# Kernel optimization log

Measured on AMD Instinct MI355X. Metric: run time of the kernel, lower is better.

## Reference

```python
import jax, jax.numpy as jnp
import numpy as np

N = 50000
E = 800000
F_IN = 128
H = 64
C = 10
BN_EPS = 1e-5


def _glorot(key, shape):
    fan_in = shape[0]
    return jax.random.normal(key, shape, dtype=jnp.float32) / jnp.sqrt(jnp.float32(fan_in))


def setup_inputs() -> dict:
    key = jax.random.key(0)
    ks = jax.random.split(key, 16)
    inp = {
        "x": jax.random.normal(ks[0], (N, F_IN), dtype=jnp.float32),
        "edge_index": jax.random.randint(ks[1], (2, E), 0, N, dtype=jnp.int64),
    }
    # GINConv layer params: eps (train_eps=True, init 0), 2-layer MLP, BN affine
    dims = [(F_IN, H), (H, H), (H, H)]
    for i, (din, dout) in enumerate(dims, start=1):
        k1, k2 = jax.random.split(ks[1 + i], 2)
        inp[f"eps{i}"] = jnp.float32(0.0)
        inp[f"w{i}a"] = _glorot(k1, (din, H))
        inp[f"b{i}a"] = jnp.zeros((H,), jnp.float32)
        inp[f"w{i}b"] = _glorot(k2, (H, H))
        inp[f"b{i}b"] = jnp.zeros((H,), jnp.float32)
        inp[f"g{i}"] = jnp.ones((H,), jnp.float32)
        inp[f"be{i}"] = jnp.zeros((H,), jnp.float32)
    inp["lin_w"] = _glorot(ks[10], (H, C))
    inp["lin_b"] = jnp.zeros((C,), jnp.float32)
    return inp


def _gin_conv(x, src, dst, eps, wa, ba, wb, bb, g, be):
    # sum-aggregate neighbor features: scatter-add x[src] into dst rows
    agg = jax.ops.segment_sum(x[src], dst, num_segments=N)
    h = (1.0 + eps) * x + agg
    # MLP: Linear-ReLU-Linear-ReLU-BatchNorm1d (training-mode batch stats)
    h = jax.nn.relu(h @ wa + ba)
    h = jax.nn.relu(h @ wb + bb)
    mean = jnp.mean(h, axis=0)
    var = jnp.var(h, axis=0)
    return (h - mean) * jax.lax.rsqrt(var + BN_EPS) * g + be


def reference(x, edge_index,
              eps1, w1a, b1a, w1b, b1b, g1, be1,
              eps2, w2a, b2a, w2b, b2b, g2, be2,
              eps3, w3a, b3a, w3b, b3b, g3, be3,
              lin_w, lin_b):
    src, dst = edge_index[0], edge_index[1]
    h = jax.nn.relu(_gin_conv(x, src, dst, eps1, w1a, b1a, w1b, b1b, g1, be1))
    h = jax.nn.relu(_gin_conv(h, src, dst, eps2, w2a, b2a, w2b, b2b, g2, be2))
    h = jax.nn.relu(_gin_conv(h, src, dst, eps3, w3a, b3a, w3b, b3b, g3, be3))
    return h @ lin_w + lin_b
```

## Files before the change

### kernel.cpp

```cpp
#include <hip/hip_runtime.h>
#include <hip/hip_fp16.h>

#define NN 50000
#define NGROUP 3125
#define NCHUNK 391
#define CHCAP 3072
#define SLAB 8192
#define BN_EPS 1e-5f

typedef unsigned int uint;
typedef unsigned short ushort;
typedef _Float16 half8 __attribute__((ext_vector_type(8)));
typedef float floatx4 __attribute__((ext_vector_type(4)));

__device__ __forceinline__ int aswz(int slot) { return slot ^ ((slot >> 4) & 7); }

__device__ __forceinline__ float h_lo(uint u) {
    return __half2float(__ushort_as_half((ushort)(u & 0xFFFFu)));
}
__device__ __forceinline__ float h_hi(uint u) {
    return __half2float(__ushort_as_half((ushort)(u >> 16)));
}
__device__ __forceinline__ void unpack8(uint4 v, float* f) {
    f[0] = h_lo(v.x); f[1] = h_hi(v.x);
    f[2] = h_lo(v.y); f[3] = h_hi(v.y);
    f[4] = h_lo(v.z); f[5] = h_hi(v.z);
    f[6] = h_lo(v.w); f[7] = h_hi(v.w);
}

__global__ __launch_bounds__(256) void sortA_kernel(
    const int* __restrict__ ei, int* __restrict__ gcur,
    uint* __restrict__ bucket, int E)
{
    __shared__ int s_hist[NCHUNK];
    __shared__ int s_offs[NCHUNK];
    __shared__ int s_cur[NCHUNK];
    __shared__ int s_gb[NCHUNK];
    __shared__ int s_scanA[512], s_scanB[512];
    __shared__ uint s_sorted[SLAB];

    const int tid  = threadIdx.x;
    const int base = blockIdx.x * SLAB;
    const int cnt  = min(SLAB, E - base);

    for (int i = tid; i < NCHUNK; i += 256) s_hist[i] = 0;
    __syncthreads();

    uint pk[SLAB / 256];
    int nloc = 0;
    for (int i = tid; i < cnt; i += 256) {
        int src = ei[base + i];
        int dst = ei[E + base + i];
        int c = dst >> 7;
        pk[nloc++] = (uint)src | ((uint)(dst & 127) << 16) | ((uint)c << 23);
        atomicAdd(&s_hist[c], 1);
    }
    __syncthreads();
    for (int i = tid; i < 512; i += 256) s_scanA[i] = (i < NCHUNK) ? s_hist[i] : 0;
    __syncthreads();
    int* sa = s_scanA; int* sb = s_scanB;
    for (int off = 1; off < 512; off <<= 1) {
        for (int i = tid; i < 512; i += 256)
            sb[i] = sa[i] + ((i >= off) ? sa[i - off] : 0);
        __syncthreads();
        int* t = sa; sa = sb; sb = t;
    }
    for (int i = tid; i < NCHUNK; i += 256) {
        int excl = sa[i] - s_hist[i];
        s_offs[i] = excl;
        s_cur[i]  = excl;
    }
    __syncthreads();
    for (int k = 0; k < nloc; k++) {
        int c = pk[k] >> 23;
        int pos = atomicAdd(&s_cur[c], 1);
        s_sorted[pos] = pk[k];
    }
    __syncthreads();
    for (int c = tid; c < NCHUNK; c += 256) {
        int n = s_hist[c];
        s_gb[c] = n ? atomicAdd(&gcur[c], n) : 0;
    }
    __syncthreads();
    for (int i = tid; i < cnt; i += 256) {
        uint v = s_sorted[i];
        int c = v >> 23;
        int li = i - s_offs[c];
        bucket[(size_t)c * CHCAP + s_gb[c] + li] = v;
    }
}

__global__ __launch_bounds__(256) void fillB_kernel(
    const uint* __restrict__ bucket, const int* __restrict__ gcur,
    int* __restrict__ rowPtr, int* __restrict__ csr_src)
{
    __shared__ int s_hist[128];
    __shared__ int s_excl[128];
    __shared__ int s_cur[128];
    __shared__ int s_ws[4];
    __shared__ int s_base;
    const int c = blockIdx.x;
    const int tid = threadIdx.x;
    const int cnt = gcur[c];
    const int row0 = c * 128;

    int part = 0;
    for (int i = tid; i < c; i += 256) part += gcur[i];
    #pragma unroll
    for (int off = 32; off >= 1; off >>= 1) part += __shfl_down(part, off, 64);
    if ((tid & 63) == 0) s_ws[tid >> 6] = part;
    if (tid < 128) s_hist[tid] = 0;
    __syncthreads();
    if (tid == 0) s_base = s_ws[0] + s_ws[1] + s_ws[2] + s_ws[3];
    __syncthreads();
    const int base = s_base;
    if (tid == 0 && c == NCHUNK - 1) rowPtr[NN] = base + cnt;

    for (int i = tid; i < cnt; i += 256) {
        uint v = bucket[(size_t)c * CHCAP + i];
        atomicAdd(&s_hist[(v >> 16) & 127], 1);
    }
    __syncthreads();
    if (tid < 128) {
        int lane = tid & 63;
        int v = s_hist[tid];
        int incl = v;
        #pragma unroll
        for (int off = 1; off < 64; off <<= 1) {
            int t = __shfl_up(incl, off, 64);
            if (lane >= off) incl += t;
        }
        s_excl[tid] = incl - v;
    }
    __syncthreads();
    if (tid < 128) {
        int excl = s_excl[tid];
        if (tid >= 64) excl += s_excl[63] + s_hist[63];
        s_cur[tid] = excl;
        int row = row0 + tid;
        if (row < NN) rowPtr[row] = base + excl;
    }
    __syncthreads();
    for (int i = tid; i < cnt; i += 256) {
        uint v = bucket[(size_t)c * CHCAP + i];
        int dl  = (v >> 16) & 127;
        int src = v & 0xFFFFu;
        int ofs = atomicAdd(&s_cur[dl], 1);
        csr_src[base + ofs] = src;
    }
}

template<int FIN, bool APPLY>
__global__ __launch_bounds__(256, 4) void proj_kernel(
    const void* __restrict__ in_v,
    const float* __restrict__ stats_in, const float* __restrict__ g_in,
    const float* __restrict__ be_in,
    const float* __restrict__ wa,
    ushort* __restrict__ y_out)
{
    constexpr int KC = FIN / 32;
    __shared__ __align__(16) _Float16 s_B[FIN * 64];
    __shared__ __align__(16) _Float16 s_Y[4][1024];

    const int tid = threadIdx.x, w = tid >> 6, lane = tid & 63;
    const int q = lane >> 4, mm = lane & 15;

    for (int i = tid; i < FIN * 64; i += 256) {
        int j = i & 7, l = (i >> 3) & 63, t = i >> 9;
        int kc = t >> 2, nt = t & 3;
        int k = kc * 32 + (l >> 4) * 8 + j;
        int n = nt * 16 + (l & 15);
        s_B[i] = (_Float16)wa[k * 64 + n];
    }

    float scv[2][8], shv[2][8];
    if (APPLY) {
        #pragma unroll
        for (int kc = 0; kc < 2; kc++)
            #pragma unroll
            for (int j = 0; j < 8; j++) {
                int c = kc * 32 + q * 8 + j;
                float mean = stats_in[c] * (1.0f / NN);
                float var  = stats_in[64 + c] * (1.0f / NN) - mean * mean;
                float rstd = rsqrtf(var + BN_EPS);
                float s    = rstd * g_in[c];
                scv[kc][j] = s;
                shv[kc][j] = be_in[c] - mean * s;
            }
    }
    __syncthreads();

    int g = blockIdx.x * 4 + w;
    if (g >= NGROUP) return;
    const int row = g * 16 + mm;

    half8 af[KC];
    if (FIN == 128) {
        const float* xin = (const float*)in_v;
        #pragma unroll
        for (int kc = 0; kc < KC; kc++) {
            const float* p = xin + (size_t)row * 128 + kc * 32 + q * 8;
            float4 a = *(const float4*)p;
            float4 b = *(const float4*)(p + 4);
            half8 hv;
            hv[0] = (_Float16)a.x; hv[1] = (_Float16)a.y;
            hv[2] = (_Float16)a.z; hv[3] = (_Float16)a.w;
            hv[4] = (_Float16)b.x; hv[5] = (_Float16)b.y;
            hv[6] = (_Float16)b.z; hv[7] = (_Float16)b.w;
            af[kc] = hv;
        }
    } else {
        const ushort* hin = (const ushort*)in_v;
        #pragma unroll
        for (int kc = 0; kc < KC; kc++) {
            uint4 vv = *(const uint4*)(hin + (size_t)row * 64 + kc * 32 + q * 8);
            float f[8]; unpack8(vv, f);
            half8 hv;
            #pragma unroll
            for (int j = 0; j < 8; j++) {
                float z = APPLY ? fmaxf(fmaf(f[j], scv[kc][j], shv[kc][j]), 0.0f) : f[j];
                hv[j] = (_Float16)z;
            }
            af[kc] = hv;
        }
    }

    floatx4 acc[4] = {};
    #pragma unroll
    for (int nt = 0; nt < 4; nt++)
        #pragma unroll
        for (int kc = 0; kc < KC; kc++) {
            half8 bf = *(const half8*)(s_B + ((size_t)(kc * 4 + nt) * 64 + lane) * 8);
            acc[nt] = __builtin_amdgcn_mfma_f32_16x16x32_f16(af[kc], bf, acc[nt], 0, 0, 0);
        }

    _Float16* s_Yw = &s_Y[w][0];
    #pragma unroll
    for (int nt = 0; nt < 4; nt++)
        #pragma unroll
        for (int r = 0; r < 4; r++)
            s_Yw[(q * 4 + r) * 64 + nt * 16 + mm] = (_Float16)acc[nt][r];
    half8 t0 = *(const half8*)(s_Yw + lane * 8);
    half8 t1 = *(const half8*)(s_Yw + 512 + lane * 8);
    half8* dst = (half8*)((_Float16*)y_out + (size_t)g * 1024);
    dst[lane] = t0;
    dst[64 + lane] = t1;
}

__global__ __launch_bounds__(512, 4) void gin_gather_kernel(
    const ushort* __restrict__ y,
    const int* __restrict__ rowPtr, const int* __restrict__ csr_src,
    const float* __restrict__ eps_p, const float* __restrict__ ba,
    const float* __restrict__ wb, const float* __restrict__ bb,
    ushort* __restrict__ h_out, float* __restrict__ stats_out)
{
    __shared__ __align__(16) _Float16 s_B2[64 * 64];
    __shared__ __align__(16) _Float16 s_A[8][1024];
    __shared__ float s_red[8][64];

    const int tid = threadIdx.x, w = tid >> 6, lane = tid & 63;
    const int cc = lane & 7, gph = lane >> 3;
    const int q = lane >> 4, mm = lane & 15;

    for (int i = tid; i < 64 * 64; i += 512) {
        int j = i & 7, l = (i >> 3) & 63, t = i >> 9;
        int kc = t >> 2, nt = t & 3;
        int k = kc * 32 + (l >> 4) * 8 + j;
        int n = nt * 16 + (l & 15);
        s_B2[i] = (_Float16)wb[k * 64 + n];
    }

    const float eps1 = 1.0f + eps_p[0];
    float bav[8];
    #pragma unroll
    for (int j = 0; j < 8; j++) bav[j] = ba[8 * cc + j];
    float bbv[4];
    #pragma unroll
    for (int nt = 0; nt < 4; nt++) bbv[nt] = bb[nt * 16 + mm];
    __syncthreads();

    float bn_s[4] = {0.f, 0.f, 0.f, 0.f};
    float bn_q[4] = {0.f, 0.f, 0.f, 0.f};
    const uint4* y4 = (const uint4*)y;
    const int g = blockIdx.x * 8 + w;

    if (g < NGROUP) {
        const int row0 = g * 16;
        _Float16* s_Aw = &s_A[w][0];

        for (int m = 0; m < 16; m += 4) {
            int e[4], en[4], s[4];
            float a[4][8];
            uint4 v[4];
            #pragma unroll
            for (int i = 0; i < 4; i++) {
                int row = row0 + m + i;
                e[i] = rowPtr[row] + gph;
                en[i] = rowPtr[row + 1];
                #pragma unroll
                for (int j = 0; j < 8; j++) a[i][j] = 0.0f;
            }
            if (gph == 0) {
                #pragma unroll
                for (int i = 0; i < 4; i++) {
                    uint4 sv = y4[(size_t)(row0 + m + i) * 8 + cc];
                    float f[8]; unpack8(sv, f);
                    #pragma unroll
                    for (int j = 0; j < 8; j++) a[i][j] = eps1 * f[j];
                }
            }
            #pragma unroll
            for (int i = 0; i < 4; i++) s[i] = (e[i] < en[i]) ? csr_src[e[i]] : -1;
            #pragma unroll
            for (int i = 0; i < 4; i++) if (s[i] >= 0) v[i] = y4[(size_t)s[i] * 8 + cc];

            int mx = max(max(s[0], s[1]), max(s[2], s[3]));
            while (mx >= 0) {
                int n[4]; uint4 p[4];
                #pragma unroll
                for (int i = 0; i < 4; i++) {
                    n[i] = -1;
                    if (s[i] >= 0) { e[i] += 8; n[i] = (e[i] < en[i]) ? csr_src[e[i]] : -1; }
                }
                #pragma unroll
                for (int i = 0; i < 4; i++) if (n[i] >= 0) p[i] = y4[(size_t)n[i] * 8 + cc];
                #pragma unroll
                for (int i = 0; i < 4; i++) {
                    if (s[i] >= 0) {
                        float f[8]; unpack8(v[i], f);
                        #pragma unroll
                        for (int j = 0; j < 8; j++) a[i][j] += f[j];
                    }
                    s[i] = n[i]; v[i] = p[i];
                }
                mx = max(max(s[0], s[1]), max(s[2], s[3]));
            }

            #pragma unroll
            for (int off = 8; off < 64; off <<= 1)
                #pragma unroll
                for (int i = 0; i < 4; i++)
                    #pragma unroll
                    for (int j = 0; j < 8; j++)
                        a[i][j] += __shfl_xor(a[i][j], off, 64);

            if (gph == 0) {
                #pragma unroll
                for (int i = 0; i < 4; i++) {
                    half8 hv;
                    #pragma unroll
                    for (int j = 0; j < 8; j++)
                        hv[j] = (_Float16)fmaxf(a[i][j] + bav[j], 0.0f);
                    int slot = (cc >> 2) * 64 + (cc & 3) * 16 + (m + i);
                    *(half8*)(s_Aw + (size_t)aswz(slot) * 8) = hv;
                }
            }
        }

        half8 af2[2];
        #pragma unroll
        for (int kc = 0; kc < 2; kc++)
            af2[kc] = *(const half8*)(s_Aw + (size_t)aswz(kc * 64 + lane) * 8);
        floatx4 acc2[4] = {};
        #pragma unroll
        for (int nt = 0; nt < 4; nt++)
            #pragma unroll
            for (int kc = 0; kc < 2; kc++) {
                half8 bf = *(const half8*)(s_B2 + ((size_t)(kc * 4 + nt) * 64 + lane) * 8);
                acc2[nt] = __builtin_amdgcn_mfma_f32_16x16x32_f16(af2[kc], bf, acc2[nt], 0, 0, 0);
            }

        #pragma unroll
        for (int nt = 0; nt < 4; nt++)
            #pragma unroll
            for (int r = 0; r < 4; r++) {
                float val = fmaxf(acc2[nt][r] + bbv[nt], 0.0f);
                bn_s[nt] += val;
                bn_q[nt] += val * val;
                s_Aw[(q * 4 + r) * 64 + nt * 16 + mm] = (_Float16)val;
            }
        half8 t0 = *(const half8*)(s_Aw + lane * 8);
        half8 t1 = *(const half8*)(s_Aw + 512 + lane * 8);
        half8* dst = (half8*)((_Float16*)h_out + (size_t)row0 * 64);
        dst[lane] = t0;
        dst[64 + lane] = t1;
    }

    #pragma unroll
    for (int nt = 0; nt < 4; nt++) {
        bn_s[nt] += __shfl_xor(bn_s[nt], 16, 64);
        bn_s[nt] += __shfl_xor(bn_s[nt], 32, 64);
        bn_q[nt] += __shfl_xor(bn_q[nt], 16, 64);
        bn_q[nt] += __shfl_xor(bn_q[nt], 32, 64);
    }
    __syncthreads();
    if (lane < 16) {
        #pragma unroll
        for (int nt = 0; nt < 4; nt++) s_red[w][nt * 16 + lane] = bn_s[nt];
    }
    __syncthreads();
    if (w == 0) {
        float s = 0;
        #pragma unroll
        for (int j = 0; j < 8; j++) s += s_red[j][lane];
        atomicAdd(&stats_out[lane], s);
    }
    __syncthreads();
    if (lane < 16) {
        #pragma unroll
        for (int nt = 0; nt < 4; nt++) s_red[w][nt * 16 + lane] = bn_q[nt];
    }
    __syncthreads();
    if (w == 0) {
        float s = 0;
        #pragma unroll
        for (int j = 0; j < 8; j++) s += s_red[j][lane];
        atomicAdd(&stats_out[64 + lane], s);
    }
}

__global__ __launch_bounds__(256) void final_linear_kernel(
    const ushort* __restrict__ h, const float* __restrict__ stats,
    const float* __restrict__ g, const float* __restrict__ be,
    const float* __restrict__ w, const float* __restrict__ b,
    float* __restrict__ out)
{
    __shared__ float s_w[640];
    __shared__ float s_b[10];
    __shared__ float s_scale[64];
    __shared__ float s_shift[64];
    for (int i = threadIdx.x; i < 640; i += 256) s_w[i] = w[i];
    if (threadIdx.x < 10) s_b[threadIdx.x] = b[threadIdx.x];
    if (threadIdx.x < 64) {
        int c = threadIdx.x;
        float mean = stats[c] * (1.0f / NN);
        float var  = stats[64 + c] * (1.0f / NN) - mean * mean;
        float rstd = rsqrtf(var + BN_EPS);
        float s    = rstd * g[c];
        s_scale[c] = s;
        s_shift[c] = be[c] - mean * s;
    }
    __syncthreads();
    int row = blockIdx.x * 256 + threadIdx.x;
    if (row >= NN) return;
    float acc[10];
    #pragma unroll
    for (int c = 0; c < 10; c++) acc[c] = s_b[c];
    const uint4* hr = (const uint4*)(h + (size_t)row * 64);
    #pragma unroll
    for (int ch = 0; ch < 8; ch++) {
        uint4 v = hr[ch];
        float f[8]; unpack8(v, f);
        #pragma unroll
        for (int j = 0; j < 8; j++) {
            int k = ch * 8 + j;
            float val = fmaxf(fmaf(f[j], s_scale[k], s_shift[k]), 0.0f);
            #pragma unroll
            for (int c = 0; c < 10; c++) acc[c] = fmaf(val, s_w[k * 10 + c], acc[c]);
        }
    }
    #pragma unroll
    for (int c = 0; c < 10; c++) out[row * 10 + c] = acc[c];
}

extern "C" void kernel_launch(void* const* d_in, const int* in_sizes, int n_in,
                              void* d_out, int out_size, void* d_ws, size_t ws_size,
                              hipStream_t stream)
{
    const float* x  = (const float*)d_in[0];
    const int*   ei = (const int*)d_in[1];
    const int E = in_sizes[1] / 2;

    const float* eps[3]; const float* wa[3]; const float* ba[3];
    const float* wb[3];  const float* bb[3]; const float* g[3]; const float* be[3];
    for (int i = 0; i < 3; i++) {
        int base = 2 + 7 * i;
        eps[i] = (const float*)d_in[base + 0];
        wa[i]  = (const float*)d_in[base + 1];
        ba[i]  = (const float*)d_in[base + 2];
        wb[i]  = (const float*)d_in[base + 3];
        bb[i]  = (const float*)d_in[base + 4];
        g[i]   = (const float*)d_in[base + 5];
        be[i]  = (const float*)d_in[base + 6];
    }
    const float* lin_w = (const float*)d_in[23];
    const float* lin_b = (const float*)d_in[24];
    float* out = (float*)d_out;

    char*  base   = (char*)d_ws;
    int*   gcur   = (int*)base;
    float* stats  = (float*)(gcur + 512);
    int*   rowPtr = (int*)(stats + 384);
    uint*  bucket = (uint*)(rowPtr + NN + 1);
    int*   csrsrc = (int*)(bucket + (size_t)NCHUNK * CHCAP);
    size_t ioff   = (char*)(csrsrc + E) - base;
    ushort* yb    = (ushort*)(base + ((ioff + 15) & ~(size_t)15));
    ushort* hA    = yb + (size_t)NN * 64;
    ushort* hB    = hA + (size_t)NN * 64;

    hipMemsetAsync(gcur, 0, (512 + 384) * sizeof(int), stream);
    sortA_kernel<<<(E + SLAB - 1) / SLAB, 256, 0, stream>>>(ei, gcur, bucket, E);
    fillB_kernel<<<NCHUNK, 256, 0, stream>>>(bucket, gcur, rowPtr, csrsrc);

    const int PB = (NGROUP + 3) / 4;
    const int GB = (NGROUP + 7) / 8;

    proj_kernel<128, false><<<PB, 256, 0, stream>>>(
        x, nullptr, nullptr, nullptr, wa[0], yb);
    gin_gather_kernel<<<GB, 512, 0, stream>>>(
        yb, rowPtr, csrsrc, eps[0], ba[0], wb[0], bb[0], hA, stats);
    proj_kernel<64, true><<<PB, 256, 0, stream>>>(
        hA, stats, g[0], be[0], wa[1], yb);
    gin_gather_kernel<<<GB, 512, 0, stream>>>(
        yb, rowPtr, csrsrc, eps[1], ba[1], wb[1], bb[1], hB, stats + 128);
    proj_kernel<64, true><<<PB, 256, 0, stream>>>(
        hB, stats + 128, g[1], be[1], wa[2], yb);
    gin_gather_kernel<<<GB, 512, 0, stream>>>(
        yb, rowPtr, csrsrc, eps[2], ba[2], wb[2], bb[2], hA, stats + 256);
    final_linear_kernel<<<(NN + 255) / 256, 256, 0, stream>>>(
        hA, stats + 256, g[2], be[2], lin_w, lin_b, out);
}
```

Before: 299.3 us.

## Unroll gather two edges deep, accumulate in packed fp16, replicate BN stat atomics

```diff
diff --git a/kernel.cpp b/kernel.cpp
--- a/kernel.cpp
+++ b/kernel.cpp
@@ -6,11 +6,13 @@
 #define NCHUNK 391
 #define CHCAP 3072
 #define SLAB 8192
+#define NREP 8
 #define BN_EPS 1e-5f
 
 typedef unsigned int uint;
 typedef unsigned short ushort;
 typedef _Float16 half8 __attribute__((ext_vector_type(8)));
+typedef _Float16 half2t __attribute__((ext_vector_type(2)));
 typedef float floatx4 __attribute__((ext_vector_type(4)));
 
 __device__ __forceinline__ int aswz(int slot) { return slot ^ ((slot >> 4) & 7); }
@@ -26,6 +28,16 @@
     f[2] = h_lo(v.y); f[3] = h_hi(v.y);
     f[4] = h_lo(v.z); f[5] = h_hi(v.z);
     f[6] = h_lo(v.w); f[7] = h_hi(v.w);
+}
+__device__ __forceinline__ uint pkadd(uint a, uint b) {
+    half2t x = __builtin_bit_cast(half2t, a);
+    half2t y = __builtin_bit_cast(half2t, b);
+    half2t r = x + y;
+    return __builtin_bit_cast(uint, r);
+}
+__device__ __forceinline__ void pkadd4(uint4& a, uint4 b) {
+    a.x = pkadd(a.x, b.x); a.y = pkadd(a.y, b.y);
+    a.z = pkadd(a.z, b.z); a.w = pkadd(a.w, b.w);
 }
 
 __global__ __launch_bounds__(256) void sortA_kernel(
@@ -180,8 +192,14 @@
             #pragma unroll
             for (int j = 0; j < 8; j++) {
                 int c = kc * 32 + q * 8 + j;
-                float mean = stats_in[c] * (1.0f / NN);
-                float var  = stats_in[64 + c] * (1.0f / NN) - mean * mean;
+                float s0 = 0.f, s1 = 0.f;
+                #pragma unroll
+                for (int r = 0; r < NREP; r++) {
+                    s0 += stats_in[r * 128 + c];
+                    s1 += stats_in[r * 128 + 64 + c];
+                }
+                float mean = s0 * (1.0f / NN);
+                float var  = s1 * (1.0f / NN) - mean * mean;
                 float rstd = rsqrtf(var + BN_EPS);
                 float s    = rstd * g_in[c];
                 scv[kc][j] = s;
@@ -289,68 +307,69 @@
         _Float16* s_Aw = &s_A[w][0];
 
         for (int m = 0; m < 16; m += 4) {
-            int e[4], en[4], s[4];
-            float a[4][8];
-            uint4 v[4];
+            int e[4], en[4], s0[4], s1[4];
+            uint4 v0[4], v1[4];
+            uint4 pk[4];
             #pragma unroll
             for (int i = 0; i < 4; i++) {
                 int row = row0 + m + i;
                 e[i] = rowPtr[row] + gph;
                 en[i] = rowPtr[row + 1];
-                #pragma unroll
-                for (int j = 0; j < 8; j++) a[i][j] = 0.0f;
-            }
-            if (gph == 0) {
+                pk[i].x = pk[i].y = pk[i].z = pk[i].w = 0u;
+            }
+            #pragma unroll
+            for (int i = 0; i < 4; i++) s0[i] = (e[i] < en[i]) ? csr_src[e[i]] : -1;
+            #pragma unroll
+            for (int i = 0; i < 4; i++) s1[i] = (e[i] + 8 < en[i]) ? csr_src[e[i] + 8] : -1;
+            #pragma unroll
+            for (int i = 0; i < 4; i++) if (s0[i] >= 0) v0[i] = y4[(size_t)s0[i] * 8 + cc];
+            #pragma unroll
+            for (int i = 0; i < 4; i++) if (s1[i] >= 0) v1[i] = y4[(size_t)s1[i] * 8 + cc];
+
+            int mx = max(max(max(s0[0], s0[1]), max(s0[2], s0[3])),
+                         max(max(s1[0], s1[1]), max(s1[2], s1[3])));
+            while (mx >= 0) {
+                int n0[4], n1[4]; uint4 p0[4], p1[4];
+                #pragma unroll
+                for (int i = 0; i < 4; i++) n0[i] = (e[i] + 16 < en[i]) ? csr_src[e[i] + 16] : -1;
+                #pragma unroll
+                for (int i = 0; i < 4; i++) n1[i] = (e[i] + 24 < en[i]) ? csr_src[e[i] + 24] : -1;
+                #pragma unroll
+                for (int i = 0; i < 4; i++) if (n0[i] >= 0) p0[i] = y4[(size_t)n0[i] * 8 + cc];
+                #pragma unroll
+                for (int i = 0; i < 4; i++) if (n1[i] >= 0) p1[i] = y4[(size_t)n1[i] * 8 + cc];
                 #pragma unroll
                 for (int i = 0; i < 4; i++) {
+                    if (s0[i] >= 0) pkadd4(pk[i], v0[i]);
+                    if (s1[i] >= 0) pkadd4(pk[i], v1[i]);
+                    e[i] += 16;
+                    s0[i] = n0[i]; v0[i] = p0[i];
+                    s1[i] = n1[i]; v1[i] = p1[i];
+                }
+                mx = max(max(max(s0[0], s0[1]), max(s0[2], s0[3])),
+                         max(max(s1[0], s1[1]), max(s1[2], s1[3])));
+            }
+
+            #pragma unroll
+            for (int i = 0; i < 4; i++) {
+                float a[8];
+                unpack8(pk[i], a);
+                if (gph == 0) {
                     uint4 sv = y4[(size_t)(row0 + m + i) * 8 + cc];
                     float f[8]; unpack8(sv, f);
                     #pragma unroll
-                    for (int j = 0; j < 8; j++) a[i][j] = eps1 * f[j];
+                    for (int j = 0; j < 8; j++) a[j] = fmaf(eps1, f[j], a[j]);
                 }
-            }
-            #pragma unroll
-            for (int i = 0; i < 4; i++) s[i] = (e[i] < en[i]) ? csr_src[e[i]] : -1;
-            #pragma unroll
-            for (int i = 0; i < 4; i++) if (s[i] >= 0) v[i] = y4[(size_t)s[i] * 8 + cc];
-
-            int mx = max(max(s[0], s[1]), max(s[2], s[3]));
-            while (mx >= 0) {
-                int n[4]; uint4 p[4];
-                #pragma unroll
-                for (int i = 0; i < 4; i++) {
-                    n[i] = -1;
-                    if (s[i] >= 0) { e[i] += 8; n[i] = (e[i] < en[i]) ? csr_src[e[i]] : -1; }
-                }
-                #pragma unroll
-                for (int i = 0; i < 4; i++) if (n[i] >= 0) p[i] = y4[(size_t)n[i] * 8 + cc];
-                #pragma unroll
-                for (int i = 0; i < 4; i++) {
-                    if (s[i] >= 0) {
-                        float f[8]; unpack8(v[i], f);
-                        #pragma unroll
-                        for (int j = 0; j < 8; j++) a[i][j] += f[j];
-                    }
-                    s[i] = n[i]; v[i] = p[i];
-                }
-                mx = max(max(s[0], s[1]), max(s[2], s[3]));
-            }
-
-            #pragma unroll
-            for (int off = 8; off < 64; off <<= 1)
-                #pragma unroll
-                for (int i = 0; i < 4; i++)
+                #pragma unroll
+                for (int off = 8; off < 64; off <<= 1)
                     #pragma unroll
                     for (int j = 0; j < 8; j++)
-                        a[i][j] += __shfl_xor(a[i][j], off, 64);
-
-            if (gph == 0) {
-                #pragma unroll
-                for (int i = 0; i < 4; i++) {
+                        a[j] += __shfl_xor(a[j], off, 64);
+                if (gph == 0) {
                     half8 hv;
                     #pragma unroll
                     for (int j = 0; j < 8; j++)
-                        hv[j] = (_Float16)fmaxf(a[i][j] + bav[j], 0.0f);
+                        hv[j] = (_Float16)fmaxf(a[j] + bav[j], 0.0f);
                     int slot = (cc >> 2) * 64 + (cc & 3) * 16 + (m + i);
                     *(half8*)(s_Aw + (size_t)aswz(slot) * 8) = hv;
                 }
@@ -403,7 +422,7 @@
         float s = 0;
         #pragma unroll
         for (int j = 0; j < 8; j++) s += s_red[j][lane];
-        atomicAdd(&stats_out[lane], s);
+        atomicAdd(&stats_out[(size_t)(blockIdx.x & (NREP - 1)) * 128 + lane], s);
     }
     __syncthreads();
     if (lane < 16) {
@@ -415,7 +434,7 @@
         float s = 0;
         #pragma unroll
         for (int j = 0; j < 8; j++) s += s_red[j][lane];
-        atomicAdd(&stats_out[64 + lane], s);
+        atomicAdd(&stats_out[(size_t)(blockIdx.x & (NREP - 1)) * 128 + 64 + lane], s);
     }
 }
 
@@ -433,8 +452,14 @@
     if (threadIdx.x < 10) s_b[threadIdx.x] = b[threadIdx.x];
     if (threadIdx.x < 64) {
         int c = threadIdx.x;
-        float mean = stats[c] * (1.0f / NN);
-        float var  = stats[64 + c] * (1.0f / NN) - mean * mean;
+        float s0 = 0.f, s1 = 0.f;
+        #pragma unroll
+        for (int r = 0; r < NREP; r++) {
+            s0 += stats[r * 128 + c];
+            s1 += stats[r * 128 + 64 + c];
+        }
+        float mean = s0 * (1.0f / NN);
+        float var  = s1 * (1.0f / NN) - mean * mean;
         float rstd = rsqrtf(var + BN_EPS);
         float s    = rstd * g[c];
         s_scale[c] = s;
@@ -490,7 +515,7 @@
     char*  base   = (char*)d_ws;
     int*   gcur   = (int*)base;
     float* stats  = (float*)(gcur + 512);
-    int*   rowPtr = (int*)(stats + 384);
+    int*   rowPtr = (int*)(stats + 3 * NREP * 128);
     uint*  bucket = (uint*)(rowPtr + NN + 1);
     int*   csrsrc = (int*)(bucket + (size_t)NCHUNK * CHCAP);
     size_t ioff   = (char*)(csrsrc + E) - base;
@@ -498,7 +523,7 @@
     ushort* hA    = yb + (size_t)NN * 64;
     ushort* hB    = hA + (size_t)NN * 64;
 
-    hipMemsetAsync(gcur, 0, (512 + 384) * sizeof(int), stream);
+    hipMemsetAsync(gcur, 0, (512 + 3 * NREP * 128) * sizeof(int), stream);
     sortA_kernel<<<(E + SLAB - 1) / SLAB, 256, 0, stream>>>(ei, gcur, bucket, E);
     fillB_kernel<<<NCHUNK, 256, 0, stream>>>(bucket, gcur, rowPtr, csrsrc);
 
@@ -512,11 +537,11 @@
     proj_kernel<64, true><<<PB, 256, 0, stream>>>(
         hA, stats, g[0], be[0], wa[1], yb);
     gin_gather_kernel<<<GB, 512, 0, stream>>>(
-        yb, rowPtr, csrsrc, eps[1], ba[1], wb[1], bb[1], hB, stats + 128);
+        yb, rowPtr, csrsrc, eps[1], ba[1], wb[1], bb[1], hB, stats + NREP * 128);
     proj_kernel<64, true><<<PB, 256, 0, stream>>>(
-        hB, stats + 128, g[1], be[1], wa[2], yb);
+        hB, stats + NREP * 128, g[1], be[1], wa[2], yb);
     gin_gather_kernel<<<GB, 512, 0, stream>>>(
-        yb, rowPtr, csrsrc, eps[2], ba[2], wb[2], bb[2], hA, stats + 256);
+        yb, rowPtr, csrsrc, eps[2], ba[2], wb[2], bb[2], hA, stats + 2 * NREP * 128);
     final_linear_kernel<<<(NN + 255) / 256, 256, 0, stream>>>(
-        hA, stats + 256, g[2], be[2], lin_w, lin_b, out);
-}
+        hA, stats + 2 * NREP * 128, g[2], be[2], lin_w, lin_b, out);
+}
```

Result: slower. 351.4 us (+17.4%).
